# Performance work log

Hardware: AMD Instinct MI355X
Metric: run time of the kernel (lower is better)

Reference implementation:

```python
import jax, jax.numpy as jnp
import numpy as np
import math

IN_FEATURES = 729   # n^2 with n = 27 = 3^3
HIDDEN = 2916
OUT_FEATURES = 729
BASE = 3
FACTOR = 0
B, D = 64, 768      # batch, channel dim (x: [B, D, IN_FEATURES])


def _butterfly_factor_to_matrix(twiddle, factor_index):
    # twiddle: (n//b, b, b) -> dense n x n butterfly factor matrix (numpy, setup-time only)
    n_div_b, b, _ = twiddle.shape
    n = b * n_div_b
    stride = b ** factor_index
    # eye(n) rearranged: 'bs (diagblk j stride)' -> (bs, diagblk, j, stride)
    x = np.eye(n, dtype=np.float32).reshape(n, n // (b * stride), b, stride)
    # twiddle rearranged: '(diagblk stride) i j' -> (diagblk, stride, i, j)
    t = twiddle.reshape(n // (b * stride), stride, b, b)
    out = np.einsum('dsij,bdjs->bdis', t, x).reshape(n, n)
    return out.T


def _sparse_mask():
    b = BASE
    log_b_n = int(math.log(math.sqrt(IN_FEATURES), b))
    n = b ** log_b_n
    twiddle = np.arange(1, n * b + 1, dtype=np.float32).reshape(n // b, b, b)
    m1 = _butterfly_factor_to_matrix(twiddle, FACTOR)
    mask = np.kron(m1, m1)
    return jnp.asarray((mask > 0).astype(np.float32))  # [729, 729] 0/1 mask


def setup_inputs() -> dict:
    key = jax.random.key(0)
    k1, k2, k3, k4 = jax.random.split(key, 4)
    x = jax.random.normal(k1, (B, D, IN_FEATURES), jnp.float32)
    w1 = jax.random.normal(k2, (HIDDEN, IN_FEATURES), jnp.float32) / math.sqrt(IN_FEATURES)
    w2 = jax.random.normal(k3, (OUT_FEATURES, HIDDEN), jnp.float32) / math.sqrt(HIDDEN)
    b2 = jax.random.normal(k4, (OUT_FEATURES,), jnp.float32) * 0.01
    return {"x": x, "w1": w1, "w2": w2, "b2": b2, "sparse_mask": _sparse_mask()}


def reference(x, w1, w2, b2, sparse_mask):
    # attn_s[s,t] = sum_d fc1.W[d,s] * fc2.W[t,d], then butterfly-masked
    attn = jnp.einsum('ds,td->st', w1, w2) * sparse_mask  # [in, out]
    out = jnp.einsum('bds,st->bdt', x, attn) + b2          # [B, D, out]
    return jax.nn.gelu(out, approximate=False)             # torch nn.GELU uses exact erf
```

## Files before the change

kernel.cpp:

```cpp
#include <hip/hip_runtime.h>
#include <hip/hip_bf16.h>


__device__ __forceinline__ float gelu_f(float v) {
    float u2 = v * v;
    float z = -1.5957691216f * v * fmaf(0.044715f, u2, 1.0f);
    float e = __expf(z);
    return v * __builtin_amdgcn_rcpf(1.0f + e);
}

__global__ void attn_zero_kernel(float* __restrict__ attn) {
    int i = blockIdx.x * 256 + threadIdx.x;
    if (i < 81 * 81) attn[i] = 0.0f;
}

#define CH 108

__global__ __launch_bounds__(256) void bfly_attn_kernel(
        const float* __restrict__ w1,
        const float* __restrict__ w2,
        float* __restrict__ attn)
{
    const int G1    = blockIdx.x % 9;
    const int d0    = (blockIdx.x / 9) * CH;
    const int tid   = threadIdx.x;

    __shared__ float ws1[CH * 81];
    __shared__ float ws2[81 * CH];

    for (int i = tid; i < CH * 81; i += 256) {
        int dl = i / 81, c = i % 81;
        ws1[i] = w1[(d0 + dl) * 729 + 81 * G1 + c];
    }
    for (int i = tid; i < 81 * CH; i += 256) {
        int tl = i / CH, dl = i % CH;
        ws2[i] = w2[(81 * G1 + tl) * 2916 + d0 + dl];
    }
    __syncthreads();

    if (tid < 243) {
        const int G2  = tid / 27;
        const int ls  = (tid % 27) / 3;
        const int lt0 = (tid % 3) * 3;
        const int s_l = 27 * (ls / 3) + 3 * G2 + (ls % 3);
        int t_l[3];
        #pragma unroll
        for (int j = 0; j < 3; ++j) {
            int lt = lt0 + j;
            t_l[j] = 27 * (lt / 3) + 3 * G2 + (lt % 3);
        }

        float a0 = 0.f, a1 = 0.f, a2 = 0.f;
        for (int dl = 0; dl < CH; ++dl) {
            float av = ws1[dl * 81 + s_l];
            a0 = fmaf(av, ws2[t_l[0] * CH + dl], a0);
            a1 = fmaf(av, ws2[t_l[1] * CH + dl], a1);
            a2 = fmaf(av, ws2[t_l[2] * CH + dl], a2);
        }

        const int g = 9 * G1 + G2;
        float* dst = &attn[g * 81 + ls * 9 + lt0];
        atomicAdd(dst + 0, a0);
        atomicAdd(dst + 1, a1);
        atomicAdd(dst + 2, a2);
    }
}

#define TILE 8
#define NV4  (TILE * 729 / 4)

struct f3 { float x, y, z; };

__global__ __launch_bounds__(256) void bfly_mlp_kernel(
        const float* __restrict__ xg,
        const float* __restrict__ attn,
        const float* __restrict__ b2g,
        float* __restrict__ outg)
{
    __shared__ float xs[TILE * 729];

    const int tid = threadIdx.x;
    const bool active = (tid < 243);

    float a[9][3], bias[3];
    int tb = 0, sb = 0;
    if (active) {
        const int t1 = tid / 9;
        const int G2 = tid % 9;
        const int G1 = t1 / 3;
        const int li = t1 % 3;
        tb = 3 * tid;
        sb = 81 * G1 + 3 * G2;
        const int g  = 9 * G1 + G2;
        #pragma unroll
        for (int ls = 0; ls < 9; ++ls) {
            f3 v = *reinterpret_cast<const f3*>(&attn[g * 81 + ls * 9 + 3 * li]);
            a[ls][0] = v.x; a[ls][1] = v.y; a[ls][2] = v.z;
        }
        f3 v = *reinterpret_cast<const f3*>(&b2g[tb]);
        bias[0] = v.x; bias[1] = v.y; bias[2] = v.z;
    }

    const long long rowbase = (long long)blockIdx.x * TILE;

    {
        const uint4* __restrict__ src = (const uint4*)(xg + rowbase * 729);
        uint4* dst = (uint4*)xs;
        #pragma unroll
        for (int k = 0; k < 6; ++k) {
            int i = tid + k * 256;
            if (i < NV4) dst[i] = src[i];
        }
    }
    __syncthreads();

    float res[TILE][3];
    if (active) {
        #pragma unroll
        for (int r = 0; r < TILE; ++r) {
            const float* xr = &xs[r * 729 + sb];
            float xv[9];
            #pragma unroll
            for (int i2 = 0; i2 < 3; ++i2)
                #pragma unroll
                for (int j2 = 0; j2 < 3; ++j2)
                    xv[3 * i2 + j2] = xr[27 * i2 + j2];

            float acc0 = bias[0], acc1 = bias[1], acc2 = bias[2];
            #pragma unroll
            for (int ls = 0; ls < 9; ++ls) {
                acc0 = fmaf(xv[ls], a[ls][0], acc0);
                acc1 = fmaf(xv[ls], a[ls][1], acc1);
                acc2 = fmaf(xv[ls], a[ls][2], acc2);
            }
            res[r][0] = gelu_f(acc0);
            res[r][1] = gelu_f(acc1);
            res[r][2] = gelu_f(acc2);
        }
    }
    __syncthreads();

    if (active) {
        #pragma unroll
        for (int r = 0; r < TILE; ++r) {
            float* o = &xs[r * 729 + tb];
            o[0] = res[r][0]; o[1] = res[r][1]; o[2] = res[r][2];
        }
    }
    __syncthreads();

    {
        uint4* __restrict__ dst = (uint4*)(outg + rowbase * 729);
        const uint4* src = (const uint4*)xs;
        #pragma unroll
        for (int k = 0; k < 6; ++k) {
            int i = tid + k * 256;
            if (i < NV4) dst[i] = src[i];
        }
    }
}

extern "C" void kernel_launch(void* const* d_in, const int* in_sizes, int n_in,
                              void* d_out, int out_size, void* d_ws, size_t ws_size,
                              hipStream_t stream) {
    const float* x  = (const float*)d_in[0];
    const float* w1 = (const float*)d_in[1];
    const float* w2 = (const float*)d_in[2];
    const float* b2 = (const float*)d_in[3];

    float* attn = (float*)d_ws;

    attn_zero_kernel<<<26, 256, 0, stream>>>(attn);
    bfly_attn_kernel<<<9 * 27, 256, 0, stream>>>(w1, w2, attn);

    const int n_rows = 64 * 768;
    bfly_mlp_kernel<<<n_rows / TILE, 256, 0, stream>>>(
        x, attn, b2, (float*)d_out);
}
```

Baseline: 279.5 us.

## Double-buffer input tiles in a persistent MLP block loop with direct output stores

The MLP kernel now runs fewer blocks, each processing four 4-row tiles. The next tile is prefetched into registers while the current one is computed, then written into a second shared buffer. Outputs are stored directly from registers as 12-byte writes instead of being staged through shared memory for coalesced 16-byte stores. This aims to overlap global loads with compute and cut barriers and LDS traffic, at the cost of less-coalesced output writes and fewer resident blocks.

```diff
diff --git a/kernel.cpp b/kernel.cpp
--- a/kernel.cpp
+++ b/kernel.cpp
@@ -66,8 +66,10 @@
     }
 }
 
-#define TILE 8
-#define NV4  (TILE * 729 / 4)
+#define TILE 4
+#define TPB  4
+#define NBLK 3072
+#define TV4  (TILE * 729 / 4)
 
 struct f3 { float x, y, z; };
 
@@ -77,7 +79,7 @@
         const float* __restrict__ b2g,
         float* __restrict__ outg)
 {
-    __shared__ float xs[TILE * 729];
+    __shared__ float xs[2][TILE * 729];
 
     const int tid = threadIdx.x;
     const bool active = (tid < 243);
@@ -101,62 +103,66 @@
         bias[0] = v.x; bias[1] = v.y; bias[2] = v.z;
     }
 
-    const long long rowbase = (long long)blockIdx.x * TILE;
+    const long long rowbase = (long long)blockIdx.x * (TILE * TPB);
+    const uint4* __restrict__ xsrc = (const uint4*)(xg + rowbase * 729);
+
+    uint4 g0, g1, g2;
+    const bool has2 = (tid + 512) < TV4;
 
     {
-        const uint4* __restrict__ src = (const uint4*)(xg + rowbase * 729);
-        uint4* dst = (uint4*)xs;
-        #pragma unroll
-        for (int k = 0; k < 6; ++k) {
-            int i = tid + k * 256;
-            if (i < NV4) dst[i] = src[i];
+        const uint4* s = xsrc;
+        g0 = s[tid];
+        g1 = s[tid + 256];
+        if (has2) g2 = s[tid + 512];
+        uint4* d = (uint4*)xs[0];
+        d[tid] = g0;
+        d[tid + 256] = g1;
+        if (has2) d[tid + 512] = g2;
+    }
+
+    int cur = 0;
+    for (int t = 0; t < TPB; ++t) {
+        __syncthreads();
+
+        if (t + 1 < TPB) {
+            const uint4* s = xsrc + (t + 1) * TV4;
+            g0 = s[tid];
+            g1 = s[tid + 256];
+            if (has2) g2 = s[tid + 512];
         }
-    }
-    __syncthreads();
 
-    float res[TILE][3];
-    if (active) {
-        #pragma unroll
-        for (int r = 0; r < TILE; ++r) {
-            const float* xr = &xs[r * 729 + sb];
-            float xv[9];
+        if (active) {
+            const float* xb = xs[cur];
             #pragma unroll
-            for (int i2 = 0; i2 < 3; ++i2)
+            for (int r = 0; r < TILE; ++r) {
+                const float* xr = xb + r * 729 + sb;
+                float xv[9];
                 #pragma unroll
-                for (int j2 = 0; j2 < 3; ++j2)
-                    xv[3 * i2 + j2] = xr[27 * i2 + j2];
+                for (int i2 = 0; i2 < 3; ++i2)
+                    #pragma unroll
+                    for (int j2 = 0; j2 < 3; ++j2)
+                        xv[3 * i2 + j2] = xr[27 * i2 + j2];
 
-            float acc0 = bias[0], acc1 = bias[1], acc2 = bias[2];
-            #pragma unroll
-            for (int ls = 0; ls < 9; ++ls) {
-                acc0 = fmaf(xv[ls], a[ls][0], acc0);
-                acc1 = fmaf(xv[ls], a[ls][1], acc1);
-                acc2 = fmaf(xv[ls], a[ls][2], acc2);
+                float acc0 = bias[0], acc1 = bias[1], acc2 = bias[2];
+                #pragma unroll
+                for (int ls = 0; ls < 9; ++ls) {
+                    acc0 = fmaf(xv[ls], a[ls][0], acc0);
+                    acc1 = fmaf(xv[ls], a[ls][1], acc1);
+                    acc2 = fmaf(xv[ls], a[ls][2], acc2);
+                }
+                f3 o; o.x = gelu_f(acc0); o.y = gelu_f(acc1); o.z = gelu_f(acc2);
+                const long long row = rowbase + (long long)t * TILE + r;
+                *reinterpret_cast<f3*>(&outg[row * 729 + tb]) = o;
             }
-            res[r][0] = gelu_f(acc0);
-            res[r][1] = gelu_f(acc1);
-            res[r][2] = gelu_f(acc2);
         }
-    }
-    __syncthreads();
 
-    if (active) {
-        #pragma unroll
-        for (int r = 0; r < TILE; ++r) {
-            float* o = &xs[r * 729 + tb];
-            o[0] = res[r][0]; o[1] = res[r][1]; o[2] = res[r][2];
+        if (t + 1 < TPB) {
+            uint4* d = (uint4*)xs[cur ^ 1];
+            d[tid] = g0;
+            d[tid + 256] = g1;
+            if (has2) d[tid + 512] = g2;
         }
-    }
-    __syncthreads();
-
-    {
-        uint4* __restrict__ dst = (uint4*)(outg + rowbase * 729);
-        const uint4* src = (const uint4*)xs;
-        #pragma unroll
-        for (int k = 0; k < 6; ++k) {
-            int i = tid + k * 256;
-            if (i < NV4) dst[i] = src[i];
-        }
+        cur ^= 1;
     }
 }
 
@@ -173,7 +179,5 @@
     attn_zero_kernel<<<26, 256, 0, stream>>>(attn);
     bfly_attn_kernel<<<9 * 27, 256, 0, stream>>>(w1, w2, attn);
 
-    const int n_rows = 64 * 768;
-    bfly_mlp_kernel<<<n_rows / TILE, 256, 0, stream>>>(
-        x, attn, b2, (float*)d_out);
+    bfly_mlp_kernel<<<NBLK, 256, 0, stream>>>(x, attn, b2, (float*)d_out);
 }
```

Result: no change. 279.6 us (+0.0%).
